# Optimization experiments

Measured on AMD Instinct MI355X. Metric: run time of the kernel, lower is better.

## Reference

```python
import jax, jax.numpy as jnp
import numpy as np
import math

B, H, S, DK = 4, 16, 2048, 64

def setup_inputs() -> dict:
    key = jax.random.key(0)
    kq, kk, kv, km = jax.random.split(key, 4)
    Q = jax.random.normal(kq, (B, H, S, DK), dtype=jnp.float32)
    K = jax.random.normal(kk, (B, H, S, DK), dtype=jnp.float32)
    V = jax.random.normal(kv, (B, H, S, DK), dtype=jnp.float32)
    # boolean mask [B, Sq, Sk]; True positions are masked out (set to -1e9)
    mask = jax.random.randint(km, (B, S, S), 0, 2).astype(jnp.bool_)
    return {"Q": Q, "K": K, "V": V, "mask": mask}

def reference(Q, K, V, mask):
    d_k = Q.shape[-1]
    # [B,H,Sq,Sk] scores
    scores = jnp.einsum('bhqd,bhkd->bhqk', Q, K) / math.sqrt(d_k)
    # mask [B,Sq,Sk] broadcasts over head dim (torch code repeats over heads)
    scores = jnp.where(mask[:, None, :, :], jnp.float32(-1e9), scores)
    attn = jax.nn.softmax(scores, axis=-1)
    out = jnp.einsum('bhqk,bhkd->bhqd', attn, V)
    return (out, attn)
```

## Files before the change

### kernel.cpp

```cpp
#include <hip/hip_runtime.h>
#include <cstdint>
#include <cstddef>

#define S_LEN 2048
#define DKD   64
#define BQ    64
#define BK    128
#define NKT   16
#define BDIM  256

typedef float f32x4 __attribute__((ext_vector_type(4)));
typedef short s16x8 __attribute__((ext_vector_type(8)));
typedef short s16x4 __attribute__((ext_vector_type(4)));
typedef unsigned int u32x4 __attribute__((ext_vector_type(4)));
typedef unsigned short u16t;
typedef unsigned long long u64t;

#define KS_OFF    0
#define KT_BYTES  (BK * DKD * 2)
#define VT_OFF    16384
#define VT_BYTES  (DKD * BK * 2)
#define PS_OFF    32768
#define PS_STRIDE 280
#define SMEM_SZ   (PS_OFF + BQ * PS_STRIDE)

__device__ __forceinline__ u16t f2bf(float f) {
  unsigned u = __builtin_bit_cast(unsigned, f);
  return (u16t)((u + 0x7FFFu + ((u >> 16) & 1u)) >> 16);
}
__device__ __forceinline__ float bf_lo(unsigned u) {
  return __builtin_bit_cast(float, u << 16);
}
__device__ __forceinline__ float bf_hi(unsigned u) {
  return __builtin_bit_cast(float, u & 0xFFFF0000u);
}

__device__ __forceinline__ void gl_lds16(const void* g, void* l) {
  typedef __attribute__((address_space(1))) void gvoid;
  typedef __attribute__((address_space(3))) void lvoid;
  __builtin_amdgcn_global_load_lds((gvoid*)(void*)g, (lvoid*)l, 16, 0, 0);
}

#define BAR_VM(N) do { asm volatile("s_waitcnt vmcnt(" #N ")\n\ts_barrier" ::: "memory"); \
                       __builtin_amdgcn_sched_barrier(0); } while (0)
#define BAR_LG()  do { asm volatile("s_waitcnt lgkmcnt(0)\n\ts_barrier" ::: "memory"); \
                       __builtin_amdgcn_sched_barrier(0); } while (0)
#define BAR_VM8() do { asm volatile("s_waitcnt vmcnt(8) lgkmcnt(0)\n\ts_barrier" ::: "memory"); \
                       __builtin_amdgcn_sched_barrier(0); } while (0)

__global__ __launch_bounds__(256)
void prologue(const unsigned char* __restrict__ Mg, const float* __restrict__ Kg,
              const float* __restrict__ Vg, u64t* __restrict__ bits,
              u16t* __restrict__ Kws, u16t* __restrict__ Vws) {
  __shared__ float scr[BK][DKD + 1];
  __shared__ int mflag_s;
  const int tid = threadIdx.x;
  const int bid = blockIdx.x;

  if (bid < 1024) {
    int f = 0;
    for (int i = tid; i < 4096; i += 256) if ((i & 3) && Mg[i]) f = 1;
    if (tid == 0) mflag_s = 0;
    __syncthreads();
    if (f) mflag_s = 1;
    __syncthreads();
    const int mstride = mflag_s ? 1 : 4;

    const int row = bid * 8 + (tid >> 5);
    const int wd  = tid & 31;
    const size_t kbase = (size_t)row * S_LEN + (size_t)wd * 64;
    u64t word = 0;
    if (mstride == 1) {
      const u64t* p = (const u64t*)(Mg + kbase);
      #pragma unroll
      for (int i = 0; i < 8; ++i) {
        u64t x = p[i];
        u64t nz = x | (x >> 4); nz |= nz >> 2; nz |= nz >> 1;
        nz &= 0x0101010101010101ull;
        word |= ((nz * 0x0102040810204080ull) >> 56) << (8 * i);
      }
    } else {
      const unsigned* p = (const unsigned*)Mg + kbase;
      #pragma unroll
      for (int i = 0; i < 64; ++i) word |= (u64t)(p[i] ? 1u : 0u) << i;
    }
    bits[(size_t)row * 32 + wd] = word;
  } else if (bid < 2048) {
    const int kb = bid - 1024;
    const float* src = Kg + (size_t)kb * (BK * DKD);
    u16t* dst = Kws + (size_t)kb * (BK * DKD);
    #pragma unroll
    for (int i = 0; i < 4; ++i) {
      int c = tid + 256 * i;
      int row = c >> 3, y = c & 7;
      int oc = y ^ (row & 7);
      const float4* s4 = (const float4*)(src + row * DKD + 8 * oc);
      float4 a = s4[0], b = s4[1];
      s16x8 h = { (short)f2bf(a.x), (short)f2bf(a.y), (short)f2bf(a.z), (short)f2bf(a.w),
                  (short)f2bf(b.x), (short)f2bf(b.y), (short)f2bf(b.z), (short)f2bf(b.w) };
      *(s16x8*)(dst + row * DKD + 8 * y) = h;
    }
  } else {
    const int vb = bid - 2048;
    const float4* src = (const float4*)(Vg + (size_t)vb * (BK * DKD));
    #pragma unroll
    for (int i = 0; i < 8; ++i) {
      int c = tid + 256 * i;
      float4 v = src[c];
      int k = c >> 4, d0 = (c & 15) * 4;
      scr[k][d0] = v.x; scr[k][d0 + 1] = v.y; scr[k][d0 + 2] = v.z; scr[k][d0 + 3] = v.w;
    }
    __syncthreads();
    u16t* dst = Vws + (size_t)vb * (DKD * BK);
    #pragma unroll
    for (int i = 0; i < 8; ++i) {
      int c = tid + 256 * i;
      int dv = c >> 5, y = c & 31;
      int k0 = 4 * (y ^ (dv & 7));
      ushort4 h = make_ushort4(f2bf(scr[k0][dv]), f2bf(scr[k0 + 1][dv]),
                               f2bf(scr[k0 + 2][dv]), f2bf(scr[k0 + 3][dv]));
      *(ushort4*)(dst + dv * BK + 4 * y) = h;
    }
  }
}

__global__ __launch_bounds__(256)
void attn_ws(const float* __restrict__ Qg, const u16t* __restrict__ Kws,
             const u16t* __restrict__ Vws, const u64t* __restrict__ bits,
             float* __restrict__ outg, float* __restrict__ attng) {
  __shared__ char smem[SMEM_SZ];
  const int tid = threadIdx.x;
  const int p = blockIdx.x;
  const int qb = (p >> 3) & 31;
  const int bh = (p & 7) + 8 * (p >> 8);
  const int b  = bh >> 4;
  const int lane = tid & 63, wv = tid >> 6;
  const int cl = lane & 15, g = lane >> 4;
  const int qrow = qb * BQ + 16 * wv + cl;
  const int swzK = (cl & 7) << 4;
  const int swzV = (cl & 7) << 3;

  const char* Kbh = (const char*)Kws + (size_t)bh * NKT * KT_BYTES;
  const char* Vbh = (const char*)Vws + (size_t)bh * NKT * VT_BYTES;
  const u64t* bitR = bits + (size_t)(b * S_LEN + qrow) * 32;
  float* attnQ = attng + ((size_t)bh * S_LEN + (size_t)qb * BQ) * S_LEN;

  s16x8 aq0, aq1;
  {
    const float* qr = Qg + ((size_t)bh * S_LEN + qrow) * DKD;
    float x[8], y[8];
    *(float4*)(x)     = *(const float4*)(qr + 8 * g);
    *(float4*)(x + 4) = *(const float4*)(qr + 8 * g + 4);
    *(float4*)(y)     = *(const float4*)(qr + 32 + 8 * g);
    *(float4*)(y + 4) = *(const float4*)(qr + 32 + 8 * g + 4);
    #pragma unroll
    for (int j = 0; j < 8; ++j) {
      aq0[j] = (short)f2bf(x[j] * 0.125f);
      aq1[j] = (short)f2bf(y[j] * 0.125f);
    }
  }

  auto stageK = [&](int kt, int off) {
    const char* src = Kbh + (size_t)kt * KT_BYTES + wv * 4096 + lane * 16;
    #pragma unroll
    for (int t = 0; t < 4; ++t)
      gl_lds16(src + t * 1024, (void*)(smem + off + wv * 4096 + t * 1024));
  };
  auto stageV = [&](int kt) {
    const char* src = Vbh + (size_t)kt * VT_BYTES + wv * 4096 + lane * 16;
    #pragma unroll
    for (int t = 0; t < 4; ++t)
      gl_lds16(src + t * 1024, (void*)(smem + VT_OFF + wv * 4096 + t * 1024));
  };

  float lsum = 0.f;
  stageK(0, KS_OFF);
  BAR_VM(0);
  for (int kt = 0; kt < NKT; ++kt) {
    const int cur = (kt & 1) ? VT_OFF : KS_OFF;
    if (kt + 1 < NKT) stageK(kt + 1, (kt & 1) ? KS_OFF : VT_OFF);
    ulonglong2 bw = *(const ulonglong2*)(bitR + 2 * kt);
    #pragma unroll
    for (int s = 0; s < 8; ++s) {
      const char* rb = smem + cur + (16 * s + cl) * 128;
      s16x8 k0 = *(const s16x8*)(rb + ((16 * g) ^ swzK));
      s16x8 k1 = *(const s16x8*)(rb + ((64 + 16 * g) ^ swzK));
      f32x4 acc = {0.f, 0.f, 0.f, 0.f};
      acc = __builtin_amdgcn_mfma_f32_16x16x32_bf16(k0, aq0, acc, 0, 0, 0);
      acc = __builtin_amdgcn_mfma_f32_16x16x32_bf16(k1, aq1, acc, 0, 0, 0);
      unsigned nib = (unsigned)(((s < 4) ? bw.x : bw.y) >> (16 * (s & 3) + 4 * g)) & 0xFu;
      #pragma unroll
      for (int r = 0; r < 4; ++r)
        lsum += ((nib >> r) & 1) ? 0.f : __expf(acc[r]);
    }
    if (kt + 1 < NKT) BAR_VM(0);
  }
  BAR_LG();
  stageK(0, KS_OFF);
  stageV(0);
  lsum += __shfl_xor(lsum, 16);
  lsum += __shfl_xor(lsum, 32);
  const float rinv = 1.f / lsum;
  BAR_VM(0);

  f32x4 accpv[4];
  #pragma unroll
  for (int db = 0; db < 4; ++db) accpv[db] = (f32x4){0.f, 0.f, 0.f, 0.f};

  for (int kt = 0; kt < NKT; ++kt) {
    ulonglong2 bw = *(const ulonglong2*)(bitR + 2 * kt);
    char* pbase = smem + PS_OFF + (16 * wv + cl) * PS_STRIDE;

    #pragma unroll
    for (int ks = 0; ks < 4; ++ks) {
      f32x4 qa[2];
      __builtin_amdgcn_s_setprio(1);
      #pragma unroll
      for (int sp = 0; sp < 2; ++sp) {
        int s = 2 * ks + sp;
        const char* rb = smem + KS_OFF + (16 * s + cl) * 128;
        s16x8 k0 = *(const s16x8*)(rb + ((16 * g) ^ swzK));
        s16x8 k1 = *(const s16x8*)(rb + ((64 + 16 * g) ^ swzK));
        f32x4 acc = {0.f, 0.f, 0.f, 0.f};
        acc = __builtin_amdgcn_mfma_f32_16x16x32_bf16(k0, aq0, acc, 0, 0, 0);
        acc = __builtin_amdgcn_mfma_f32_16x16x32_bf16(k1, aq1, acc, 0, 0, 0);
        qa[sp] = acc;
      }
      __builtin_amdgcn_s_setprio(0);
      unsigned hw[4];
      #pragma unroll
      for (int sp = 0; sp < 2; ++sp) {
        int s = 2 * ks + sp;
        unsigned nib = (unsigned)(((s < 4) ? bw.x : bw.y) >> (16 * (s & 3) + 4 * g)) & 0xFu;
        #pragma unroll
        for (int rr = 0; rr < 2; ++rr) {
          float p0 = ((nib >> (2 * rr)) & 1)     ? 0.f : __expf(qa[sp][2 * rr]) * rinv;
          float p1 = ((nib >> (2 * rr + 1)) & 1) ? 0.f : __expf(qa[sp][2 * rr + 1]) * rinv;
          hw[2 * sp + rr] = (unsigned)f2bf(p0) | ((unsigned)f2bf(p1) << 16);
        }
      }
      *(uint2*)(pbase + 64 * ks + 8 * g)      = make_uint2(hw[0], hw[1]);
      *(uint2*)(pbase + 64 * ks + 32 + 8 * g) = make_uint2(hw[2], hw[3]);
      s16x8 pa = __builtin_bit_cast(s16x8, (u32x4){hw[0], hw[1], hw[2], hw[3]});
      __builtin_amdgcn_s_setprio(1);
      #pragma unroll
      for (int db = 0; db < 4; ++db) {
        const char* vrow = smem + VT_OFF + (16 * db + cl) * 256;
        s16x4 v0 = *(const s16x4*)(vrow + ((64 * ks + 8 * g) ^ swzV));
        s16x4 v1 = *(const s16x4*)(vrow + ((64 * ks + 32 + 8 * g) ^ swzV));
        s16x8 vb = __builtin_shufflevector(v0, v1, 0, 1, 2, 3, 4, 5, 6, 7);
        accpv[db] = __builtin_amdgcn_mfma_f32_16x16x32_bf16(pa, vb, accpv[db], 0, 0, 0);
      }
      __builtin_amdgcn_s_setprio(0);
    }

    BAR_LG();

    if (kt + 1 < NKT) { stageK(kt + 1, KS_OFF); stageV(kt + 1); }

    #pragma unroll
    for (int i = 0; i < 4; ++i) {
      int c = tid + 256 * i;
      int q = c >> 4, ch = c & 15;
      u32x4 d = *(const u32x4*)(smem + PS_OFF + q * PS_STRIDE + ch * 16);
      f32x4 lo = { bf_lo(d.x), bf_hi(d.x), bf_lo(d.y), bf_hi(d.y) };
      f32x4 hi = { bf_lo(d.z), bf_hi(d.z), bf_lo(d.w), bf_hi(d.w) };
      float* dst = attnQ + (size_t)q * S_LEN + kt * BK + ch * 8;
      __builtin_nontemporal_store(lo, (f32x4*)dst);
      __builtin_nontemporal_store(hi, (f32x4*)(dst + 4));
    }

    if (kt + 1 < NKT) BAR_VM8();
  }

  const int q0 = qb * BQ + 16 * wv + 4 * g;
  #pragma unroll
  for (int r = 0; r < 4; ++r) {
    float* orow = outg + (size_t)(bh * S_LEN + q0 + r) * DKD + cl;
    #pragma unroll
    for (int db = 0; db < 4; ++db) orow[16 * db] = accpv[db][r];
  }
}

#define FB_KSTR 144
#define FB_VOFF (BK * FB_KSTR)
#define FB_VSTR 272
#define FB_POFF (FB_VOFF + DKD * FB_VSTR)
#define FB_SMEM (FB_POFF + BQ * FB_VSTR)

__global__ __launch_bounds__(256)
void attn_fb(const float* __restrict__ Qg, const float* __restrict__ Kg,
             const float* __restrict__ Vg, const unsigned char* __restrict__ Mg,
             float* __restrict__ outg, float* __restrict__ attng) {
  __shared__ char smem[FB_SMEM];
  __shared__ int mflag_s;
  const int tid = threadIdx.x;
  const int p = blockIdx.x;
  const int qb = (p >> 3) & 31;
  const int bh = (p & 7) + 8 * (p >> 8);
  const int b  = bh >> 4;

  int f = 0;
  for (int i = tid; i < 4096; i += BDIM) if ((i & 3) && Mg[i]) f = 1;
  if (tid == 0) mflag_s = 0;
  __syncthreads();
  if (f) mflag_s = 1;
  __syncthreads();
  const int mstride = mflag_s ? 1 : 4;

  const int lane = tid & 63, wv = tid >> 6;
  const int cl = lane & 15, g = lane >> 4;
  const int q0 = qb * BQ + 16 * wv + 4 * g;

  const float* Kbh = Kg + (size_t)bh * S_LEN * DKD;
  const float* Vbh = Vg + (size_t)bh * S_LEN * DKD;

  float* aRow[4]; float* oRow[4]; const unsigned char* mRow[4];
  #pragma unroll
  for (int r = 0; r < 4; ++r) {
    aRow[r] = attng + (size_t)(bh * S_LEN + q0 + r) * S_LEN + cl;
    oRow[r] = outg + (size_t)(bh * S_LEN + q0 + r) * DKD + cl;
    mRow[r] = Mg + ((size_t)(b * S_LEN + q0 + r) * S_LEN + cl) * (size_t)mstride;
  }

  s16x8 aq0, aq1;
  {
    const float* qrow = Qg + ((size_t)bh * S_LEN + qb * BQ + 16 * wv + cl) * DKD;
    float x[8], y[8];
    *(float4*)(x)     = *(const float4*)(qrow + 8 * g);
    *(float4*)(x + 4) = *(const float4*)(qrow + 8 * g + 4);
    *(float4*)(y)     = *(const float4*)(qrow + 32 + 8 * g);
    *(float4*)(y + 4) = *(const float4*)(qrow + 32 + 8 * g + 4);
    #pragma unroll
    for (int j = 0; j < 8; ++j) { aq0[j] = (short)f2bf(x[j]); aq1[j] = (short)f2bf(y[j]); }
  }

  float lsum[4] = {0.f, 0.f, 0.f, 0.f};
  for (int kt = 0; kt < NKT; ++kt) {
    const float4* ksrc = (const float4*)(Kbh + (size_t)kt * (BK * DKD));
    #pragma unroll
    for (int it = 0; it < 8; ++it) {
      int c = tid + BDIM * it;
      float4 v = ksrc[c];
      *(ushort4*)(smem + (c >> 4) * FB_KSTR + (c & 15) * 8) =
          make_ushort4(f2bf(v.x), f2bf(v.y), f2bf(v.z), f2bf(v.w));
    }
    __syncthreads();
    #pragma unroll
    for (int s = 0; s < 8; ++s) {
      s16x8 b0 = *(const s16x8*)(smem + (16 * s + cl) * FB_KSTR + 16 * g);
      s16x8 b1 = *(const s16x8*)(smem + (16 * s + cl) * FB_KSTR + 64 + 16 * g);
      f32x4 acc = {0.f, 0.f, 0.f, 0.f};
      acc = __builtin_amdgcn_mfma_f32_16x16x32_bf16(aq0, b0, acc, 0, 0, 0);
      acc = __builtin_amdgcn_mfma_f32_16x16x32_bf16(aq1, b1, acc, 0, 0, 0);
      #pragma unroll
      for (int r = 0; r < 4; ++r) {
        bool mk = mRow[r][(size_t)(kt * BK + 16 * s) * mstride] != 0;
        lsum[r] += mk ? 0.f : __expf(acc[r] * 0.125f);
      }
    }
    __syncthreads();
  }
  float rinv[4];
  #pragma unroll
  for (int r = 0; r < 4; ++r) {
    float l = lsum[r];
    #pragma unroll
    for (int d = 1; d < 16; d <<= 1) l += __shfl_xor(l, d);
    rinv[r] = 1.f / l;
  }

  f32x4 accpv[4];
  #pragma unroll
  for (int db = 0; db < 4; ++db) accpv[db] = (f32x4){0.f, 0.f, 0.f, 0.f};

  for (int kt = 0; kt < NKT; ++kt) {
    const float4* ksrc = (const float4*)(Kbh + (size_t)kt * (BK * DKD));
    #pragma unroll
    for (int it = 0; it < 8; ++it) {
      int c = tid + BDIM * it;
      float4 v = ksrc[c];
      *(ushort4*)(smem + (c >> 4) * FB_KSTR + (c & 15) * 8) =
          make_ushort4(f2bf(v.x), f2bf(v.y), f2bf(v.z), f2bf(v.w));
    }
    const float4* vsrc = (const float4*)(Vbh + (size_t)kt * (BK * DKD));
    #pragma unroll
    for (int it = 0; it < 8; ++it) {
      int c = tid + BDIM * it;
      float4 v = vsrc[c];
      int k = c >> 4, d0 = (c & 15) * 4;
      *(u16t*)(smem + FB_VOFF + (d0 + 0) * FB_VSTR + k * 2) = f2bf(v.x);
      *(u16t*)(smem + FB_VOFF + (d0 + 1) * FB_VSTR + k * 2) = f2bf(v.y);
      *(u16t*)(smem + FB_VOFF + (d0 + 2) * FB_VSTR + k * 2) = f2bf(v.z);
      *(u16t*)(smem + FB_VOFF + (d0 + 3) * FB_VSTR + k * 2) = f2bf(v.w);
    }
    __syncthreads();

    #pragma unroll
    for (int ks = 0; ks < 4; ++ks) {
      f32x4 qa[2];
      #pragma unroll
      for (int sp = 0; sp < 2; ++sp) {
        int s = 2 * ks + sp;
        s16x8 b0 = *(const s16x8*)(smem + (16 * s + cl) * FB_KSTR + 16 * g);
        s16x8 b1 = *(const s16x8*)(smem + (16 * s + cl) * FB_KSTR + 64 + 16 * g);
        f32x4 acc = {0.f, 0.f, 0.f, 0.f};
        acc = __builtin_amdgcn_mfma_f32_16x16x32_bf16(aq0, b0, acc, 0, 0, 0);
        acc = __builtin_amdgcn_mfma_f32_16x16x32_bf16(aq1, b1, acc, 0, 0, 0);
        qa[sp] = acc;
      }
      #pragma unroll
      for (int sp = 0; sp < 2; ++sp) {
        int s = 2 * ks + sp;
        #pragma unroll
        for (int r = 0; r < 4; ++r) {
          bool mk = mRow[r][(size_t)(kt * BK + 16 * s) * mstride] != 0;
          float pv = mk ? 0.f : __expf(qa[sp][r] * 0.125f) * rinv[r];
          __builtin_nontemporal_store(pv, aRow[r] + kt * BK + 16 * s);
          *(u16t*)(smem + FB_POFF + (16 * wv + 4 * g + r) * FB_VSTR +
                   (32 * ks + 16 * sp + cl) * 2) = f2bf(pv);
        }
      }
      s16x4 p0 = *(const s16x4*)(smem + FB_POFF + (16 * wv + cl) * FB_VSTR + (32 * ks + 4 * g) * 2);
      s16x4 p1 = *(const s16x4*)(smem + FB_POFF + (16 * wv + cl) * FB_VSTR + (32 * ks + 16 + 4 * g) * 2);
      s16x8 pa = __builtin_shufflevector(p0, p1, 0, 1, 2, 3, 4, 5, 6, 7);
      #pragma unroll
      for (int db = 0; db < 4; ++db) {
        s16x4 v0 = *(const s16x4*)(smem + FB_VOFF + (16 * db + cl) * FB_VSTR + (32 * ks + 4 * g) * 2);
        s16x4 v1 = *(const s16x4*)(smem + FB_VOFF + (16 * db + cl) * FB_VSTR + (32 * ks + 16 + 4 * g) * 2);
        s16x8 vb = __builtin_shufflevector(v0, v1, 0, 1, 2, 3, 4, 5, 6, 7);
        accpv[db] = __builtin_amdgcn_mfma_f32_16x16x32_bf16(pa, vb, accpv[db], 0, 0, 0);
      }
    }
    __syncthreads();
  }

  #pragma unroll
  for (int db = 0; db < 4; ++db)
    #pragma unroll
    for (int r = 0; r < 4; ++r)
      oRow[r][16 * db] = accpv[db][r];
}

extern "C" void kernel_launch(void* const* d_in, const int* in_sizes, int n_in,
                              void* d_out, int out_size, void* d_ws, size_t ws_size,
                              hipStream_t stream) {
  const float* Q = (const float*)d_in[0];
  const float* K = (const float*)d_in[1];
  const float* V = (const float*)d_in[2];
  const unsigned char* M = (const unsigned char*)d_in[3];
  float* out = (float*)d_out;
  float* attn = out + (size_t)4 * 16 * S_LEN * DKD;

  const size_t BITS_SZ = (size_t)4 * S_LEN * 32 * 8;
  const size_t KWS_SZ  = (size_t)64 * NKT * BK * DKD * 2;
  const size_t VWS_SZ  = (size_t)64 * NKT * DKD * BK * 2;
  if (ws_size >= BITS_SZ + KWS_SZ + VWS_SZ) {
    u64t* bits = (u64t*)d_ws;
    u16t* Kws = (u16t*)((char*)d_ws + BITS_SZ);
    u16t* Vws = (u16t*)((char*)d_ws + BITS_SZ + KWS_SZ);
    prologue<<<3072, 256, 0, stream>>>(M, K, V, bits, Kws, Vws);
    attn_ws<<<2048, BDIM, 0, stream>>>(Q, Kws, Vws, bits, out, attn);
  } else {
    attn_fb<<<2048, BDIM, 0, stream>>>(Q, K, V, M, out, attn);
  }
}
```

Measured before the change: 338.2 us.

## Split row-sum pass by key slice per wave to drop per-tile barriers

In the first pass, which computes the softmax denominator, each wave now covers only its own 32-key slice of the staged K tile, for all 64 query rows. Before, every wave covered all 128 keys for just its 16 rows. Since each wave only reads the part of LDS it loaded itself, the per-tile s_barrier is replaced by a plain vmcnt wait, and redundant LDS reads of K are cut. In exchange, the per-row partial sums now need a cross-wave reduction through shared memory, and each wave keeps the Q fragments for all four query groups in registers.

```diff
diff --git a/kernel.cpp b/kernel.cpp
--- a/kernel.cpp
+++ b/kernel.cpp
@@ -47,6 +47,8 @@
                        __builtin_amdgcn_sched_barrier(0); } while (0)
 #define BAR_VM8() do { asm volatile("s_waitcnt vmcnt(8) lgkmcnt(0)\n\ts_barrier" ::: "memory"); \
                        __builtin_amdgcn_sched_barrier(0); } while (0)
+#define WAIT_VM(N) do { asm volatile("s_waitcnt vmcnt(" #N ")" ::: "memory"); \
+                        __builtin_amdgcn_sched_barrier(0); } while (0)
 
 __global__ __launch_bounds__(256)
 void prologue(const unsigned char* __restrict__ Mg, const float* __restrict__ Kg,
@@ -145,9 +147,10 @@
   const u64t* bitR = bits + (size_t)(b * S_LEN + qrow) * 32;
   float* attnQ = attng + ((size_t)bh * S_LEN + (size_t)qb * BQ) * S_LEN;
 
-  s16x8 aq0, aq1;
-  {
-    const float* qr = Qg + ((size_t)bh * S_LEN + qrow) * DKD;
+  s16x8 aqp0[4], aqp1[4];
+  #pragma unroll
+  for (int qg = 0; qg < 4; ++qg) {
+    const float* qr = Qg + ((size_t)bh * S_LEN + qb * BQ + 16 * qg + cl) * DKD;
     float x[8], y[8];
     *(float4*)(x)     = *(const float4*)(qr + 8 * g);
     *(float4*)(x + 4) = *(const float4*)(qr + 8 * g + 4);
@@ -155,10 +158,14 @@
     *(float4*)(y + 4) = *(const float4*)(qr + 32 + 8 * g + 4);
     #pragma unroll
     for (int j = 0; j < 8; ++j) {
-      aq0[j] = (short)f2bf(x[j] * 0.125f);
-      aq1[j] = (short)f2bf(y[j] * 0.125f);
-    }
-  }
+      aqp0[qg][j] = (short)f2bf(x[j] * 0.125f);
+      aqp1[qg][j] = (short)f2bf(y[j] * 0.125f);
+    }
+  }
+  const u64t* bitQ[4];
+  #pragma unroll
+  for (int qg = 0; qg < 4; ++qg)
+    bitQ[qg] = bits + (size_t)(b * S_LEN + qb * BQ + 16 * qg + cl) * 32;
 
   auto stageK = [&](int kt, int off) {
     const char* src = Kbh + (size_t)kt * KT_BYTES + wv * 4096 + lane * 16;
@@ -173,34 +180,56 @@
       gl_lds16(src + t * 1024, (void*)(smem + VT_OFF + wv * 4096 + t * 1024));
   };
 
-  float lsum = 0.f;
+  float lsum4[4] = {0.f, 0.f, 0.f, 0.f};
   stageK(0, KS_OFF);
-  BAR_VM(0);
   for (int kt = 0; kt < NKT; ++kt) {
     const int cur = (kt & 1) ? VT_OFF : KS_OFF;
-    if (kt + 1 < NKT) stageK(kt + 1, (kt & 1) ? KS_OFF : VT_OFF);
-    ulonglong2 bw = *(const ulonglong2*)(bitR + 2 * kt);
-    #pragma unroll
-    for (int s = 0; s < 8; ++s) {
-      const char* rb = smem + cur + (16 * s + cl) * 128;
+    if (kt + 1 < NKT) {
+      stageK(kt + 1, (kt & 1) ? KS_OFF : VT_OFF);
+      WAIT_VM(4);
+    } else {
+      WAIT_VM(0);
+    }
+    u64t bwq[4];
+    #pragma unroll
+    for (int qg = 0; qg < 4; ++qg) bwq[qg] = bitQ[qg][2 * kt + (wv >> 1)];
+    const int bsh = 32 * (wv & 1);
+
+    #pragma unroll
+    for (int h = 0; h < 2; ++h) {
+      const char* rb = smem + cur + (32 * wv + 16 * h + cl) * 128;
       s16x8 k0 = *(const s16x8*)(rb + ((16 * g) ^ swzK));
       s16x8 k1 = *(const s16x8*)(rb + ((64 + 16 * g) ^ swzK));
-      f32x4 acc = {0.f, 0.f, 0.f, 0.f};
-      acc = __builtin_amdgcn_mfma_f32_16x16x32_bf16(k0, aq0, acc, 0, 0, 0);
-      acc = __builtin_amdgcn_mfma_f32_16x16x32_bf16(k1, aq1, acc, 0, 0, 0);
-      unsigned nib = (unsigned)(((s < 4) ? bw.x : bw.y) >> (16 * (s & 3) + 4 * g)) & 0xFu;
-      #pragma unroll
-      for (int r = 0; r < 4; ++r)
-        lsum += ((nib >> r) & 1) ? 0.f : __expf(acc[r]);
-    }
-    if (kt + 1 < NKT) BAR_VM(0);
-  }
-  BAR_LG();
+      #pragma unroll
+      for (int qg = 0; qg < 4; ++qg) {
+        f32x4 acc = {0.f, 0.f, 0.f, 0.f};
+        acc = __builtin_amdgcn_mfma_f32_16x16x32_bf16(k0, aqp0[qg], acc, 0, 0, 0);
+        acc = __builtin_amdgcn_mfma_f32_16x16x32_bf16(k1, aqp1[qg], acc, 0, 0, 0);
+        unsigned nib = (unsigned)(bwq[qg] >> (bsh + 16 * h + 4 * g)) & 0xFu;
+        #pragma unroll
+        for (int r = 0; r < 4; ++r)
+          lsum4[qg] += ((nib >> r) & 1) ? 0.f : __expf(acc[r]);
+      }
+    }
+  }
   stageK(0, KS_OFF);
   stageV(0);
-  lsum += __shfl_xor(lsum, 16);
-  lsum += __shfl_xor(lsum, 32);
-  const float rinv = 1.f / lsum;
+  #pragma unroll
+  for (int qg = 0; qg < 4; ++qg) {
+    lsum4[qg] += __shfl_xor(lsum4[qg], 16);
+    lsum4[qg] += __shfl_xor(lsum4[qg], 32);
+  }
+  float* red = (float*)(smem + PS_OFF);
+  if (g == 0) {
+    #pragma unroll
+    for (int qg = 0; qg < 4; ++qg) red[(wv * 4 + qg) * 16 + cl] = lsum4[qg];
+  }
+  BAR_LG();
+  float tot = red[(0 * 4 + wv) * 16 + cl] + red[(1 * 4 + wv) * 16 + cl] +
+              red[(2 * 4 + wv) * 16 + cl] + red[(3 * 4 + wv) * 16 + cl];
+  const float rinv = 1.f / tot;
+  s16x8 aq0 = (wv == 0) ? aqp0[0] : (wv == 1) ? aqp0[1] : (wv == 2) ? aqp0[2] : aqp0[3];
+  s16x8 aq1 = (wv == 0) ? aqp1[0] : (wv == 1) ? aqp1[1] : (wv == 2) ? aqp1[2] : aqp1[3];
   BAR_VM(0);
 
   f32x4 accpv[4];
```

Result: slower. 379.4 us (+12.2%).

## Triple-buffer K tiles in stats pass, prefetch mask bits, use native exp2

Applied to the files above, without the earlier changes.

Folds log2(e) into the Q scale so softmax exponentials can use the raw v_exp_f32 (exp2) instruction instead of __expf. The first (row-sum) pass now rotates K tiles through three LDS regions (including the P scratch area) with a prefetch distance of two and a partial vmcnt wait. Mask-bit words are loaded one iteration ahead in both passes. This is meant to hide global-load latency and trim exp instruction overhead. The cost is added register pressure and reuse of the P buffer region during the first pass.

```diff
diff --git a/kernel.cpp b/kernel.cpp
--- a/kernel.cpp
+++ b/kernel.cpp
@@ -24,6 +24,8 @@
 #define PS_STRIDE 280
 #define SMEM_SZ   (PS_OFF + BQ * PS_STRIDE)
 
+#define QSC 0.18033688011112042f
+
 __device__ __forceinline__ u16t f2bf(float f) {
   unsigned u = __builtin_bit_cast(unsigned, f);
   return (u16t)((u + 0x7FFFu + ((u >> 16) & 1u)) >> 16);
@@ -33,6 +35,11 @@
 }
 __device__ __forceinline__ float bf_hi(unsigned u) {
   return __builtin_bit_cast(float, u & 0xFFFF0000u);
+}
+__device__ __forceinline__ float fexp2(float x) {
+  float r;
+  asm("v_exp_f32 %0, %1" : "=v"(r) : "v"(x));
+  return r;
 }
 
 __device__ __forceinline__ void gl_lds16(const void* g, void* l) {
@@ -47,6 +54,7 @@
                        __builtin_amdgcn_sched_barrier(0); } while (0)
 #define BAR_VM8() do { asm volatile("s_waitcnt vmcnt(8) lgkmcnt(0)\n\ts_barrier" ::: "memory"); \
                        __builtin_amdgcn_sched_barrier(0); } while (0)
+#define SB0()     __builtin_amdgcn_sched_barrier(0)
 
 __global__ __launch_bounds__(256)
 void prologue(const unsigned char* __restrict__ Mg, const float* __restrict__ Kg,
@@ -155,8 +163,8 @@
     *(float4*)(y + 4) = *(const float4*)(qr + 32 + 8 * g + 4);
     #pragma unroll
     for (int j = 0; j < 8; ++j) {
-      aq0[j] = (short)f2bf(x[j] * 0.125f);
-      aq1[j] = (short)f2bf(y[j] * 0.125f);
+      aq0[j] = (short)f2bf(x[j] * QSC);
+      aq1[j] = (short)f2bf(y[j] * QSC);
     }
   }
 
@@ -174,15 +182,16 @@
   };
 
   float lsum = 0.f;
+  ulonglong2 bw = *(const ulonglong2*)(bitR);
+  SB0();
   stageK(0, KS_OFF);
-  BAR_VM(0);
+  stageK(1, VT_OFF);
+  int oc = KS_OFF, o1 = VT_OFF, o2 = PS_OFF;
   for (int kt = 0; kt < NKT; ++kt) {
-    const int cur = (kt & 1) ? VT_OFF : KS_OFF;
-    if (kt + 1 < NKT) stageK(kt + 1, (kt & 1) ? KS_OFF : VT_OFF);
-    ulonglong2 bw = *(const ulonglong2*)(bitR + 2 * kt);
+    if (kt + 1 < NKT) BAR_VM(4); else BAR_VM(0);
     #pragma unroll
     for (int s = 0; s < 8; ++s) {
-      const char* rb = smem + cur + (16 * s + cl) * 128;
+      const char* rb = smem + oc + (16 * s + cl) * 128;
       s16x8 k0 = *(const s16x8*)(rb + ((16 * g) ^ swzK));
       s16x8 k1 = *(const s16x8*)(rb + ((64 + 16 * g) ^ swzK));
       f32x4 acc = {0.f, 0.f, 0.f, 0.f};
@@ -191,11 +200,18 @@
       unsigned nib = (unsigned)(((s < 4) ? bw.x : bw.y) >> (16 * (s & 3) + 4 * g)) & 0xFu;
       #pragma unroll
       for (int r = 0; r < 4; ++r)
-        lsum += ((nib >> r) & 1) ? 0.f : __expf(acc[r]);
-    }
-    if (kt + 1 < NKT) BAR_VM(0);
+        lsum += ((nib >> r) & 1) ? 0.f : fexp2(acc[r]);
+    }
+    if (kt + 1 < NKT) {
+      bw = *(const ulonglong2*)(bitR + 2 * (kt + 1));
+      SB0();
+      if (kt + 2 < NKT) stageK(kt + 2, o2);
+    }
+    int t = oc; oc = o1; o1 = o2; o2 = t;
   }
   BAR_LG();
+  bw = *(const ulonglong2*)(bitR);
+  SB0();
   stageK(0, KS_OFF);
   stageV(0);
   lsum += __shfl_xor(lsum, 16);
@@ -208,7 +224,6 @@
   for (int db = 0; db < 4; ++db) accpv[db] = (f32x4){0.f, 0.f, 0.f, 0.f};
 
   for (int kt = 0; kt < NKT; ++kt) {
-    ulonglong2 bw = *(const ulonglong2*)(bitR + 2 * kt);
     char* pbase = smem + PS_OFF + (16 * wv + cl) * PS_STRIDE;
 
     #pragma unroll
@@ -234,8 +249,8 @@
         unsigned nib = (unsigned)(((s < 4) ? bw.x : bw.y) >> (16 * (s & 3) + 4 * g)) & 0xFu;
         #pragma unroll
         for (int rr = 0; rr < 2; ++rr) {
-          float p0 = ((nib >> (2 * rr)) & 1)     ? 0.f : __expf(qa[sp][2 * rr]) * rinv;
-          float p1 = ((nib >> (2 * rr + 1)) & 1) ? 0.f : __expf(qa[sp][2 * rr + 1]) * rinv;
+          float p0 = ((nib >> (2 * rr)) & 1)     ? 0.f : fexp2(qa[sp][2 * rr]) * rinv;
+          float p1 = ((nib >> (2 * rr + 1)) & 1) ? 0.f : fexp2(qa[sp][2 * rr + 1]) * rinv;
           hw[2 * sp + rr] = (unsigned)f2bf(p0) | ((unsigned)f2bf(p1) << 16);
         }
       }
@@ -256,7 +271,13 @@
 
     BAR_LG();
 
-    if (kt + 1 < NKT) { stageK(kt + 1, KS_OFF); stageV(kt + 1); }
+    if (kt + 1 < NKT) {
+      stageK(kt + 1, KS_OFF);
+      stageV(kt + 1);
+      SB0();
+      bw = *(const ulonglong2*)(bitR + 2 * (kt + 1));
+      SB0();
+    }
 
     #pragma unroll
     for (int i = 0; i < 4; ++i) {
```

After: 410.4 us. 21.3% more time.
